# Performance work log

Measured on AMD Instinct MI355X. Metric: run time of the kernel, lower is better.

## Reference

```python
import jax, jax.numpy as jnp
import numpy as np

B, LQ, LK = 8, 256, 256
Q_SIZE = K_SIZE = H = D_V = 256
MASK_VALUE = -1000000.0


def setup_inputs() -> dict:
    key = jax.random.key(0)
    kq, kk, kv, kl, kwq, kwk, kwv = jax.random.split(key, 7)
    # Linear weights, torch nn.Linear stores (out, in); init ~ U(-1/sqrt(in), 1/sqrt(in))
    def lin(k, out_f, in_f):
        bound = 1.0 / np.sqrt(in_f)
        return jax.random.uniform(k, (out_f, in_f), jnp.float32, -bound, bound)
    return {
        "queries": jax.random.normal(kq, (B, LQ, Q_SIZE), jnp.float32),
        "keyes": jax.random.normal(kk, (B, LK, K_SIZE), jnp.float32),
        "values": jax.random.normal(kv, (B, LK, D_V), jnp.float32),
        "valid_lens": jax.random.randint(kl, (B,), 1, LK + 1),
        "W_q": lin(kwq, H, Q_SIZE),
        "W_k": lin(kwk, H, K_SIZE),
        "W_v": lin(kwv, 1, H),
    }


def reference(queries, keyes, values, valid_lens, W_q, W_k, W_v):
    # Projections (nn.Linear without bias): x @ W.T
    q = jnp.einsum("bqd,hd->bqh", queries, W_q)            # (B, Lq, H)
    k = jnp.einsum("bkd,hd->bkh", keyes, W_k)              # (B, Lk, H)
    # Broadcast-add + tanh: (B, Lq, Lk, H)
    features = jnp.tanh(q[:, :, None, :] + k[:, None, :, :])
    # W_v reduction H -> 1, squeeze: scores (B, Lq, Lk)
    scores = jnp.einsum("bqkh,h->bqk", features, W_v[0])
    # sequence_mask over the last (key) axis with value -1e6
    lk = scores.shape[-1]
    mask = jnp.arange(lk)[None, None, :] < valid_lens[:, None, None]  # (B,1,Lk)
    scores = jnp.where(mask, scores, MASK_VALUE)
    # NOTE: this repo's masked_softmax normalizes over dim=1 (the query axis),
    # faithfully reproduced here.
    attention_weights = jax.nn.softmax(scores, axis=1)
    # dropout is identity in eval / p=0.0
    return jnp.einsum("bqk,bkd->bqd", attention_weights, values)
```

## Files before the change

### kernel.cpp

```cpp
#include <hip/hip_runtime.h>

typedef float vf4 __attribute__((ext_vector_type(4)));

#define LOG2E 1.4426950408889634f
#define TWO_LOG2E 2.8853900817779268f

__device__ __forceinline__ float fexp2(float x) { return __builtin_amdgcn_exp2f(x); }
__device__ __forceinline__ float frcp(float x) { return __builtin_amdgcn_rcpf(x); }

__global__ __launch_bounds__(256) void proj_kernel(
    const float* __restrict__ queries, const float* __restrict__ keyes,
    const float* __restrict__ Wq, const float* __restrict__ Wk,
    float* __restrict__ QpH, float* __restrict__ KpH,
    float* __restrict__ Rsum) {
  __shared__ alignas(16) float At[16 * 68];
  __shared__ alignas(16) float Bt[16 * 68];
  const int t = threadIdx.x;
  if (blockIdx.x == 0 && blockIdx.y == 0 && blockIdx.z == 0) {
    *(vf4*)&Rsum[t * 8] = (vf4){0.f, 0.f, 0.f, 0.f};
    *(vf4*)&Rsum[t * 8 + 4] = (vf4){0.f, 0.f, 0.f, 0.f};
  }
  const int m0 = blockIdx.x * 64;
  const int n0 = blockIdx.y * 64;
  const int k0 = blockIdx.z * 128;
  const bool isQ = (m0 < 2048);
  const float* X = isQ ? queries : keyes;
  const float* W = isQ ? Wq : Wk;
  float* C = (isQ ? QpH : KpH) + blockIdx.z * 524288;
  const int mb = isQ ? m0 : (m0 - 2048);

  const int lm = t >> 2;
  const int lq = t & 3;
  const int mm4 = (t & 15) * 4;
  const int nn4 = (t >> 4) * 4;

  float acc[4][4] = {};
  for (int kc = k0; kc < k0 + 128; kc += 16) {
    __syncthreads();
    vf4 xa = *(const vf4*)&X[(mb + lm) * 256 + kc + lq * 4];
    vf4 wb = *(const vf4*)&W[(n0 + lm) * 256 + kc + lq * 4];
#pragma unroll
    for (int c = 0; c < 4; ++c) {
      At[(lq * 4 + c) * 68 + lm] = xa[c];
      Bt[(lq * 4 + c) * 68 + lm] = wb[c];
    }
    __syncthreads();
#pragma unroll
    for (int kk = 0; kk < 16; ++kk) {
      vf4 a4 = *(const vf4*)&At[kk * 68 + mm4];
      vf4 b4 = *(const vf4*)&Bt[kk * 68 + nn4];
#pragma unroll
      for (int i = 0; i < 4; ++i)
#pragma unroll
        for (int j = 0; j < 4; ++j) acc[i][j] += a4[i] * b4[j];
    }
  }
#pragma unroll
  for (int i = 0; i < 4; ++i) {
    vf4 o = {fexp2(acc[i][0] * TWO_LOG2E), fexp2(acc[i][1] * TWO_LOG2E),
             fexp2(acc[i][2] * TWO_LOG2E), fexp2(acc[i][3] * TWO_LOG2E)};
    *(vf4*)&C[(mb + mm4 + i) * 256 + n0 + nn4] = o;
  }
}

__global__ __launch_bounds__(256) void scores_exp_kernel(
    const float* __restrict__ QpH, const float* __restrict__ KpH,
    const float* __restrict__ Wv, const int* __restrict__ valid_lens,
    float* __restrict__ E, float* __restrict__ Rsum) {
  __shared__ alignas(16) float Qs[32 * 32];
  __shared__ alignas(16) float Ks[32 * 32];
  __shared__ alignas(16) float wvs[256];
  const int t = threadIdx.x;
  const int i0 = blockIdx.x * 32;
  const int j0 = blockIdx.y * 32;
  const int b = blockIdx.z;
  const int ti = t & 15;
  const int tj = t >> 4;

  float Swv;
  {
    vf4 w4 = *(const vf4*)&Wv[(t & 63) * 4];
    float sw = w4[0] + w4[1] + w4[2] + w4[3];
#pragma unroll
    for (int off = 1; off < 64; off <<= 1) sw += __shfl_xor(sw, off, 64);
    Swv = sw;
  }
  if (t < 64) *(vf4*)&wvs[t * 4] = *(const vf4*)&Wv[t * 4];

  const int srow = t >> 3;
  const int scg = t & 7;
  const int swcol = ((scg ^ (srow & 7)) << 2);
  const int qxor = ti & 7;
  const int kxor = tj & 7;

  float acc[2][2] = {};
  for (int hc = 0; hc < 8; ++hc) {
    __syncthreads();
    const int qoff = (((b << 8) + i0 + srow) << 8) + hc * 32 + scg * 4;
    const int koff = (((b << 8) + j0 + srow) << 8) + hc * 32 + scg * 4;
    vf4 qv = *(const vf4*)&QpH[qoff];
    vf4 qv2 = *(const vf4*)&QpH[524288 + qoff];
    vf4 kv = *(const vf4*)&KpH[koff];
    vf4 kv2 = *(const vf4*)&KpH[524288 + koff];
    *(vf4*)&Qs[srow * 32 + swcol] = qv * qv2;
    *(vf4*)&Ks[srow * 32 + swcol] = kv * kv2;
    __syncthreads();
#pragma unroll
    for (int hh = 0; hh < 8; ++hh) {
      vf4 q0 = *(const vf4*)&Qs[ti * 32 + ((hh ^ qxor) << 2)];
      vf4 q1 = *(const vf4*)&Qs[(ti + 16) * 32 + ((hh ^ qxor) << 2)];
      vf4 k0 = *(const vf4*)&Ks[tj * 32 + ((hh ^ kxor) << 2)];
      vf4 k1 = *(const vf4*)&Ks[(tj + 16) * 32 + ((hh ^ kxor) << 2)];
      vf4 wv4 = *(const vf4*)&wvs[hc * 32 + hh * 4];
#pragma unroll
      for (int e = 0; e < 4; ++e) {
        const float we = wv4[e];
        acc[0][0] += we * frcp(__builtin_fmaf(q0[e], k0[e], 1.0f));
        acc[0][1] += we * frcp(__builtin_fmaf(q0[e], k1[e], 1.0f));
        acc[1][0] += we * frcp(__builtin_fmaf(q1[e], k0[e], 1.0f));
        acc[1][1] += we * frcp(__builtin_fmaf(q1[e], k1[e], 1.0f));
      }
    }
  }

  const int len = valid_lens[b];
#pragma unroll
  for (int c = 0; c < 2; ++c) {
    const int j = j0 + tj + 16 * c;
    const bool masked = (j >= len);
    float ev[2];
#pragma unroll
    for (int r = 0; r < 2; ++r) {
      const int i = i0 + ti + 16 * r;
      const float score = Swv - 2.0f * acc[r][c];
      ev[r] = masked ? 1.0f : fexp2(score * LOG2E);
      E[(((b << 8) + j) << 8) + i] = ev[r];
    }
    float s = ev[0] + ev[1];
#pragma unroll
    for (int off = 1; off < 16; off <<= 1) s += __shfl_xor(s, off, 64);
    if (ti == 0) atomicAdd(&Rsum[(b << 8) + j], s);
  }
}

__global__ __launch_bounds__(256) void out_kernel(
    const float* __restrict__ E, const float* __restrict__ Rsum,
    const float* __restrict__ V, float* __restrict__ out) {
  __shared__ alignas(16) float As[32 * 36];
  __shared__ alignas(16) float Bs[32 * 68];
  const int t = threadIdx.x;
  const int i0 = blockIdx.x * 32;
  const int d0 = blockIdx.y * 64;
  const int b = blockIdx.z;
  const int ti = t & 15;
  const int td = t >> 4;
  const int sr = t >> 3;
  const int sc4 = (t & 7) * 4;

  float acc[2][4] = {};
  for (int jc = 0; jc < 8; ++jc) {
    const int jb = jc * 32;
    __syncthreads();
    const float rj = frcp(Rsum[(b << 8) + jb + sr]);
    {
      vf4 a = *(const vf4*)&E[(((b << 8) + jb + sr) << 8) + i0 + sc4];
      *(vf4*)&As[sr * 36 + sc4] = a * rj;
    }
#pragma unroll
    for (int s = 0; s < 2; ++s) {
      const int col = sc4 + s * 32;
      *(vf4*)&Bs[sr * 68 + col] =
          *(const vf4*)&V[(((b << 8) + jb + sr) << 8) + d0 + col];
    }
    __syncthreads();
#pragma unroll
    for (int j = 0; j < 32; ++j) {
      const float a0 = As[j * 36 + ti];
      const float a1 = As[j * 36 + ti + 16];
      vf4 b4 = *(const vf4*)&Bs[j * 68 + td * 4];
#pragma unroll
      for (int c = 0; c < 4; ++c) {
        acc[0][c] += a0 * b4[c];
        acc[1][c] += a1 * b4[c];
      }
    }
  }
#pragma unroll
  for (int r = 0; r < 2; ++r) {
    vf4 o = {acc[r][0], acc[r][1], acc[r][2], acc[r][3]};
    *(vf4*)&out[(((b << 8) + i0 + ti + 16 * r) << 8) + d0 + td * 4] = o;
  }
}

extern "C" void kernel_launch(void* const* d_in, const int* in_sizes, int n_in,
                              void* d_out, int out_size, void* d_ws, size_t ws_size,
                              hipStream_t stream) {
  const float* queries = (const float*)d_in[0];
  const float* keyes = (const float*)d_in[1];
  const float* values = (const float*)d_in[2];
  const int* valid_lens = (const int*)d_in[3];
  const float* Wq = (const float*)d_in[4];
  const float* Wk = (const float*)d_in[5];
  const float* Wv = (const float*)d_in[6];
  float* out = (float*)d_out;

  float* QpH = (float*)d_ws;
  float* KpH = QpH + 2 * 524288;
  float* E = KpH + 2 * 524288;
  float* Rsum = E + 524288;

  proj_kernel<<<dim3(64, 4, 2), 256, 0, stream>>>(queries, keyes, Wq, Wk,
                                                  QpH, KpH, Rsum);
  scores_exp_kernel<<<dim3(8, 8, 8), 256, 0, stream>>>(QpH, KpH, Wv,
                                                       valid_lens, E, Rsum);
  out_kernel<<<dim3(8, 4, 8), 256, 0, stream>>>(E, Rsum, values, out);
}
```

Measured before the change: 111.5 us.

## Enlarge per-thread tiles across kernels and split output GEMM over key chunks

The projection kernel now runs 128 threads, each computing an 8x4 tile, and the scores kernel widens its query tile to 64 rows so each thread computes 4x2 scores. Both changes raise register reuse and cut LDS reads per FMA. The output GEMM is split along the key axis into four partial products, giving more blocks with bigger per-thread tiles, and a separate reduction kernel sums them. This adds a launch, an extra workspace buffer and extra global traffic for the partials, and fewer threads per block in the projection kernel may lower occupancy.

```diff
diff --git a/kernel.cpp b/kernel.cpp
--- a/kernel.cpp
+++ b/kernel.cpp
@@ -8,7 +8,7 @@
 __device__ __forceinline__ float fexp2(float x) { return __builtin_amdgcn_exp2f(x); }
 __device__ __forceinline__ float frcp(float x) { return __builtin_amdgcn_rcpf(x); }
 
-__global__ __launch_bounds__(256) void proj_kernel(
+__global__ __launch_bounds__(128) void proj_kernel(
     const float* __restrict__ queries, const float* __restrict__ keyes,
     const float* __restrict__ Wq, const float* __restrict__ Wk,
     float* __restrict__ QpH, float* __restrict__ KpH,
@@ -17,8 +17,9 @@
   __shared__ alignas(16) float Bt[16 * 68];
   const int t = threadIdx.x;
   if (blockIdx.x == 0 && blockIdx.y == 0 && blockIdx.z == 0) {
-    *(vf4*)&Rsum[t * 8] = (vf4){0.f, 0.f, 0.f, 0.f};
-    *(vf4*)&Rsum[t * 8 + 4] = (vf4){0.f, 0.f, 0.f, 0.f};
+#pragma unroll
+    for (int s = 0; s < 4; ++s)
+      *(vf4*)&Rsum[t * 16 + s * 4] = (vf4){0.f, 0.f, 0.f, 0.f};
   }
   const int m0 = blockIdx.x * 64;
   const int n0 = blockIdx.y * 64;
@@ -29,37 +30,45 @@
   float* C = (isQ ? QpH : KpH) + blockIdx.z * 524288;
   const int mb = isQ ? m0 : (m0 - 2048);
 
-  const int lm = t >> 2;
-  const int lq = t & 3;
-  const int mm4 = (t & 15) * 4;
-  const int nn4 = (t >> 4) * 4;
-
-  float acc[4][4] = {};
+  const int srow = t >> 1;
+  const int skq = (t & 1) * 8;
+  const int tm = t & 7;
+  const int tn = t >> 3;
+
+  float acc[8][4] = {};
   for (int kc = k0; kc < k0 + 128; kc += 16) {
     __syncthreads();
-    vf4 xa = *(const vf4*)&X[(mb + lm) * 256 + kc + lq * 4];
-    vf4 wb = *(const vf4*)&W[(n0 + lm) * 256 + kc + lq * 4];
+    const float* xs = &X[(mb + srow) * 256 + kc + skq];
+    const float* ws = &W[(n0 + srow) * 256 + kc + skq];
+    vf4 xa0 = *(const vf4*)xs, xa1 = *(const vf4*)(xs + 4);
+    vf4 wb0 = *(const vf4*)ws, wb1 = *(const vf4*)(ws + 4);
 #pragma unroll
     for (int c = 0; c < 4; ++c) {
-      At[(lq * 4 + c) * 68 + lm] = xa[c];
-      Bt[(lq * 4 + c) * 68 + lm] = wb[c];
+      At[(skq + c) * 68 + srow] = xa0[c];
+      At[(skq + 4 + c) * 68 + srow] = xa1[c];
+      Bt[(skq + c) * 68 + srow] = wb0[c];
+      Bt[(skq + 4 + c) * 68 + srow] = wb1[c];
     }
     __syncthreads();
 #pragma unroll
     for (int kk = 0; kk < 16; ++kk) {
-      vf4 a4 = *(const vf4*)&At[kk * 68 + mm4];
-      vf4 b4 = *(const vf4*)&Bt[kk * 68 + nn4];
+      vf4 a0 = *(const vf4*)&At[kk * 68 + tm * 8];
+      vf4 a1 = *(const vf4*)&At[kk * 68 + tm * 8 + 4];
+      vf4 b4 = *(const vf4*)&Bt[kk * 68 + tn * 4];
 #pragma unroll
       for (int i = 0; i < 4; ++i)
 #pragma unroll
-        for (int j = 0; j < 4; ++j) acc[i][j] += a4[i] * b4[j];
-    }
-  }
-#pragma unroll
-  for (int i = 0; i < 4; ++i) {
+        for (int j = 0; j < 4; ++j) {
+          acc[i][j] += a0[i] * b4[j];
+          acc[4 + i][j] += a1[i] * b4[j];
+        }
+    }
+  }
+#pragma unroll
+  for (int i = 0; i < 8; ++i) {
     vf4 o = {fexp2(acc[i][0] * TWO_LOG2E), fexp2(acc[i][1] * TWO_LOG2E),
              fexp2(acc[i][2] * TWO_LOG2E), fexp2(acc[i][3] * TWO_LOG2E)};
-    *(vf4*)&C[(mb + mm4 + i) * 256 + n0 + nn4] = o;
+    *(vf4*)&C[(mb + tm * 8 + i) * 256 + n0 + tn * 4] = o;
   }
 }
 
@@ -67,11 +76,11 @@
     const float* __restrict__ QpH, const float* __restrict__ KpH,
     const float* __restrict__ Wv, const int* __restrict__ valid_lens,
     float* __restrict__ E, float* __restrict__ Rsum) {
-  __shared__ alignas(16) float Qs[32 * 32];
+  __shared__ alignas(16) float Qs[64 * 32];
   __shared__ alignas(16) float Ks[32 * 32];
   __shared__ alignas(16) float wvs[256];
   const int t = threadIdx.x;
-  const int i0 = blockIdx.x * 32;
+  const int i0 = blockIdx.x * 64;
   const int j0 = blockIdx.y * 32;
   const int b = blockIdx.z;
   const int ti = t & 15;
@@ -87,38 +96,44 @@
   }
   if (t < 64) *(vf4*)&wvs[t * 4] = *(const vf4*)&Wv[t * 4];
 
-  const int srow = t >> 3;
-  const int scg = t & 7;
-  const int swcol = ((scg ^ (srow & 7)) << 2);
-  const int qxor = ti & 7;
+  const int qi = t >> 2;
+  const int qg = (t & 3) * 2;
+  const int ki = t >> 3;
+  const int kg = t & 7;
+  const int rxor = ti & 7;
   const int kxor = tj & 7;
 
-  float acc[2][2] = {};
+  float acc[4][2] = {};
   for (int hc = 0; hc < 8; ++hc) {
     __syncthreads();
-    const int qoff = (((b << 8) + i0 + srow) << 8) + hc * 32 + scg * 4;
-    const int koff = (((b << 8) + j0 + srow) << 8) + hc * 32 + scg * 4;
-    vf4 qv = *(const vf4*)&QpH[qoff];
-    vf4 qv2 = *(const vf4*)&QpH[524288 + qoff];
-    vf4 kv = *(const vf4*)&KpH[koff];
-    vf4 kv2 = *(const vf4*)&KpH[524288 + koff];
-    *(vf4*)&Qs[srow * 32 + swcol] = qv * qv2;
-    *(vf4*)&Ks[srow * 32 + swcol] = kv * kv2;
+    {
+      const int qoff = (((b << 8) + i0 + qi) << 8) + hc * 32 + qg * 4;
+      vf4 q1 = *(const vf4*)&QpH[qoff] * *(const vf4*)&QpH[524288 + qoff];
+      vf4 q2 = *(const vf4*)&QpH[qoff + 4] * *(const vf4*)&QpH[524288 + qoff + 4];
+      *(vf4*)&Qs[qi * 32 + ((qg ^ (qi & 7)) << 2)] = q1;
+      *(vf4*)&Qs[qi * 32 + (((qg + 1) ^ (qi & 7)) << 2)] = q2;
+      const int koff = (((b << 8) + j0 + ki) << 8) + hc * 32 + kg * 4;
+      vf4 kv = *(const vf4*)&KpH[koff] * *(const vf4*)&KpH[524288 + koff];
+      *(vf4*)&Ks[ki * 32 + ((kg ^ (ki & 7)) << 2)] = kv;
+    }
     __syncthreads();
 #pragma unroll
     for (int hh = 0; hh < 8; ++hh) {
-      vf4 q0 = *(const vf4*)&Qs[ti * 32 + ((hh ^ qxor) << 2)];
-      vf4 q1 = *(const vf4*)&Qs[(ti + 16) * 32 + ((hh ^ qxor) << 2)];
+      vf4 wv4 = *(const vf4*)&wvs[hc * 32 + hh * 4];
       vf4 k0 = *(const vf4*)&Ks[tj * 32 + ((hh ^ kxor) << 2)];
       vf4 k1 = *(const vf4*)&Ks[(tj + 16) * 32 + ((hh ^ kxor) << 2)];
-      vf4 wv4 = *(const vf4*)&wvs[hc * 32 + hh * 4];
+      vf4 q[4];
+#pragma unroll
+      for (int r = 0; r < 4; ++r)
+        q[r] = *(const vf4*)&Qs[(ti + 16 * r) * 32 + ((hh ^ rxor) << 2)];
 #pragma unroll
       for (int e = 0; e < 4; ++e) {
         const float we = wv4[e];
-        acc[0][0] += we * frcp(__builtin_fmaf(q0[e], k0[e], 1.0f));
-        acc[0][1] += we * frcp(__builtin_fmaf(q0[e], k1[e], 1.0f));
-        acc[1][0] += we * frcp(__builtin_fmaf(q1[e], k0[e], 1.0f));
-        acc[1][1] += we * frcp(__builtin_fmaf(q1[e], k1[e], 1.0f));
+#pragma unroll
+        for (int r = 0; r < 4; ++r) {
+          acc[r][0] += we * frcp(__builtin_fmaf(q[r][e], k0[e], 1.0f));
+          acc[r][1] += we * frcp(__builtin_fmaf(q[r][e], k1[e], 1.0f));
+        }
       }
     }
   }
@@ -128,68 +143,77 @@
   for (int c = 0; c < 2; ++c) {
     const int j = j0 + tj + 16 * c;
     const bool masked = (j >= len);
-    float ev[2];
-#pragma unroll
-    for (int r = 0; r < 2; ++r) {
-      const int i = i0 + ti + 16 * r;
+    float s = 0.f;
+#pragma unroll
+    for (int r = 0; r < 4; ++r) {
       const float score = Swv - 2.0f * acc[r][c];
-      ev[r] = masked ? 1.0f : fexp2(score * LOG2E);
-      E[(((b << 8) + j) << 8) + i] = ev[r];
-    }
-    float s = ev[0] + ev[1];
+      const float ev = masked ? 1.0f : fexp2(score * LOG2E);
+      E[(((b << 8) + j) << 8) + i0 + ti + 16 * r] = ev;
+      s += ev;
+    }
 #pragma unroll
     for (int off = 1; off < 16; off <<= 1) s += __shfl_xor(s, off, 64);
     if (ti == 0) atomicAdd(&Rsum[(b << 8) + j], s);
   }
 }
 
-__global__ __launch_bounds__(256) void out_kernel(
+__global__ __launch_bounds__(256) void out_part_kernel(
     const float* __restrict__ E, const float* __restrict__ Rsum,
-    const float* __restrict__ V, float* __restrict__ out) {
-  __shared__ alignas(16) float As[32 * 36];
+    const float* __restrict__ V, float* __restrict__ O4) {
+  __shared__ alignas(16) float As[32 * 68];
   __shared__ alignas(16) float Bs[32 * 68];
   const int t = threadIdx.x;
-  const int i0 = blockIdx.x * 32;
+  const int i0 = (blockIdx.x & 3) * 64;
+  const int js = blockIdx.x >> 2;
   const int d0 = blockIdx.y * 64;
   const int b = blockIdx.z;
   const int ti = t & 15;
   const int td = t >> 4;
   const int sr = t >> 3;
-  const int sc4 = (t & 7) * 4;
-
-  float acc[2][4] = {};
-  for (int jc = 0; jc < 8; ++jc) {
-    const int jb = jc * 32;
+  const int sc8 = (t & 7) * 8;
+
+  float acc[4][4] = {};
+  for (int jc = 0; jc < 2; ++jc) {
+    const int jb = js * 64 + jc * 32;
     __syncthreads();
     const float rj = frcp(Rsum[(b << 8) + jb + sr]);
     {
-      vf4 a = *(const vf4*)&E[(((b << 8) + jb + sr) << 8) + i0 + sc4];
-      *(vf4*)&As[sr * 36 + sc4] = a * rj;
-    }
-#pragma unroll
-    for (int s = 0; s < 2; ++s) {
-      const int col = sc4 + s * 32;
-      *(vf4*)&Bs[sr * 68 + col] =
-          *(const vf4*)&V[(((b << 8) + jb + sr) << 8) + d0 + col];
+      const int eoff = (((b << 8) + jb + sr) << 8) + i0 + sc8;
+      vf4 a0 = *(const vf4*)&E[eoff] * rj;
+      vf4 a1 = *(const vf4*)&E[eoff + 4] * rj;
+      *(vf4*)&As[sr * 68 + sc8] = a0;
+      *(vf4*)&As[sr * 68 + sc8 + 4] = a1;
+      const int voff = (((b << 8) + jb + sr) << 8) + d0 + sc8;
+      *(vf4*)&Bs[sr * 68 + sc8] = *(const vf4*)&V[voff];
+      *(vf4*)&Bs[sr * 68 + sc8 + 4] = *(const vf4*)&V[voff + 4];
     }
     __syncthreads();
 #pragma unroll
     for (int j = 0; j < 32; ++j) {
-      const float a0 = As[j * 36 + ti];
-      const float a1 = As[j * 36 + ti + 16];
+      vf4 a4 = *(const vf4*)&As[j * 68 + ti * 4];
       vf4 b4 = *(const vf4*)&Bs[j * 68 + td * 4];
 #pragma unroll
-      for (int c = 0; c < 4; ++c) {
-        acc[0][c] += a0 * b4[c];
-        acc[1][c] += a1 * b4[c];
-      }
-    }
-  }
-#pragma unroll
-  for (int r = 0; r < 2; ++r) {
+      for (int r = 0; r < 4; ++r)
+#pragma unroll
+        for (int c = 0; c < 4; ++c) acc[r][c] += a4[r] * b4[c];
+    }
+  }
+  float* O = O4 + js * 524288;
+#pragma unroll
+  for (int r = 0; r < 4; ++r) {
     vf4 o = {acc[r][0], acc[r][1], acc[r][2], acc[r][3]};
-    *(vf4*)&out[(((b << 8) + i0 + ti + 16 * r) << 8) + d0 + td * 4] = o;
-  }
+    *(vf4*)&O[(((b << 8) + i0 + ti * 4 + r) << 8) + d0 + td * 4] = o;
+  }
+}
+
+__global__ __launch_bounds__(256) void out_sum_kernel(
+    const float* __restrict__ O4, float* __restrict__ out) {
+  const int idx = (blockIdx.x * 256 + threadIdx.x) * 4;
+  vf4 s = *(const vf4*)&O4[idx];
+  s += *(const vf4*)&O4[524288 + idx];
+  s += *(const vf4*)&O4[2 * 524288 + idx];
+  s += *(const vf4*)&O4[3 * 524288 + idx];
+  *(vf4*)&out[idx] = s;
 }
 
 extern "C" void kernel_launch(void* const* d_in, const int* in_sizes, int n_in,
@@ -208,10 +232,12 @@
   float* KpH = QpH + 2 * 524288;
   float* E = KpH + 2 * 524288;
   float* Rsum = E + 524288;
-
-  proj_kernel<<<dim3(64, 4, 2), 256, 0, stream>>>(queries, keyes, Wq, Wk,
+  float* O4 = Rsum + 2048;
+
+  proj_kernel<<<dim3(64, 4, 2), 128, 0, stream>>>(queries, keyes, Wq, Wk,
                                                   QpH, KpH, Rsum);
-  scores_exp_kernel<<<dim3(8, 8, 8), 256, 0, stream>>>(QpH, KpH, Wv,
+  scores_exp_kernel<<<dim3(4, 8, 8), 256, 0, stream>>>(QpH, KpH, Wv,
                                                        valid_lens, E, Rsum);
-  out_kernel<<<dim3(8, 4, 8), 256, 0, stream>>>(E, Rsum, values, out);
-}
+  out_part_kernel<<<dim3(16, 4, 8), 256, 0, stream>>>(E, Rsum, values, O4);
+  out_sum_kernel<<<512, 256, 0, stream>>>(O4, out);
+}
```

Result: slower. 122.0 us (+9.4%).
